# Optimization experiments

Hardware: AMD Instinct MI355X
Metric: run time of the kernel (lower is better)

The kernel has to match this reference:

```python
import jax, jax.numpy as jnp
import numpy as np

D_MODEL = 1024
NUM_HEADS = 16
HEAD_DIM = D_MODEL // NUM_HEADS
MAX_SEQ = 512


def rope_tables(seq_len, dim):
    inv_freq = 1.0 / (10000.0 ** (jnp.arange(0, dim, 2, dtype=jnp.float32) / dim))
    t = jnp.arange(seq_len, dtype=jnp.float32)
    freqs = jnp.einsum('i,j->ij', t, inv_freq)        # [S, dim/2]
    emb = jnp.concatenate([freqs, freqs], axis=-1)    # [S, dim]
    return jnp.cos(emb), jnp.sin(emb)


def rotate_half(x):
    x1, x2 = jnp.split(x, 2, axis=-1)
    return jnp.concatenate([-x2, x1], axis=-1)


def setup_inputs() -> dict:
    key = jax.random.key(0)
    ks = jax.random.split(key, 12)
    B, S, D = 16, 512, D_MODEL
    s = 1.0 / np.sqrt(D)
    inp = {
        'query': jax.random.normal(ks[0], (B, S, D), jnp.float32),
        'key': jax.random.normal(ks[1], (B, S, D), jnp.float32),
        'value': jax.random.normal(ks[2], (B, S, D), jnp.float32),
        'Wq': jax.random.normal(ks[3], (D, D), jnp.float32) * s,
        'bq': jnp.zeros((D,), jnp.float32),
        'Wk': jax.random.normal(ks[4], (D, D), jnp.float32) * s,
        'bk': jnp.zeros((D,), jnp.float32),
        'Wv': jax.random.normal(ks[5], (D, D), jnp.float32) * s,
        'bv': jnp.zeros((D,), jnp.float32),
        'Wo': jax.random.normal(ks[6], (D, D), jnp.float32) * s,
        'bo': jnp.zeros((D,), jnp.float32),
    }
    return inp


def reference(query, key, value, Wq, bq, Wk, bk, Wv, bv, Wo, bo):
    B, S, D = query.shape
    H, Hd = NUM_HEADS, HEAD_DIM
    scale = Hd ** -0.5

    def proj(x, W, b):  # torch Linear: x @ W.T + b -> [B,H,S,Hd]
        y = jnp.einsum('bsd,ed->bse', x, W) + b
        return y.reshape(B, S, H, Hd).transpose(0, 2, 1, 3)

    q = proj(query, Wq, bq)
    k = proj(key, Wk, bk)
    v = proj(value, Wv, bv)

    cos, sin = rope_tables(S, Hd)           # [S, Hd]
    cos = cos[None, None]                    # [1,1,S,Hd]
    sin = sin[None, None]
    q = q * cos + rotate_half(q) * sin
    k = k * cos + rotate_half(k) * sin

    attn = jnp.einsum('bhqd,bhkd->bhqk', q, k) * scale
    attn_w = jax.nn.softmax(attn, axis=-1)
    out = jnp.einsum('bhqk,bhkd->bhqd', attn_w, v)
    out = out.transpose(0, 2, 1, 3).reshape(B, S, D)
    out = jnp.einsum('bsd,ed->bse', out, Wo) + bo
    return out
```

## Files before the change

kernel.cpp:

```cpp
#include <hip/hip_runtime.h>
#include <hip/hip_bf16.h>
#include <math.h>

typedef __attribute__((ext_vector_type(8))) short short8;
typedef __attribute__((ext_vector_type(4))) float f32x4;
typedef unsigned short ushort;
typedef unsigned int uint;

#define BATCH 16
#define SEQ 512
#define DMODEL 1024
#define NHEADS 16
#define HD 64
#define MTOT (BATCH * SEQ)
#define NBUF ((size_t)MTOT * DMODEL)
#define WBUF ((size_t)DMODEL * DMODEL)

#define SZA (256 * 64)
#define SZB (128 * 64)

__device__ __forceinline__ ushort f2bf(float f) {
    union { float f; uint i; } v; v.f = f;
    uint r = v.i + 0x7fffu + ((v.i >> 16) & 1u);
    return (ushort)(r >> 16);
}

__device__ __forceinline__ short8 cvt8(float4 a, float4 b) {
    short8 r;
    r[0] = (short)f2bf(a.x); r[1] = (short)f2bf(a.y);
    r[2] = (short)f2bf(a.z); r[3] = (short)f2bf(a.w);
    r[4] = (short)f2bf(b.x); r[5] = (short)f2bf(b.y);
    r[6] = (short)f2bf(b.z); r[7] = (short)f2bf(b.w);
    return r;
}

__device__ __forceinline__ void gld16(const ushort* g, ushort* l) {
    __builtin_amdgcn_global_load_lds(
        (const __attribute__((address_space(1))) void*)g,
        (__attribute__((address_space(3))) void*)l, 16, 0, 0);
}

__device__ __forceinline__ f32x4 mfma16(short8 a, short8 b, f32x4 c) {
    return __builtin_amdgcn_mfma_f32_16x16x32_bf16(a, b, c, 0, 0, 0);
}

__global__ void fill_const(float* __restrict__ out, float val) {
    out[blockIdx.x * 256 + threadIdx.x] = val;
}

__global__ __launch_bounds__(256) void cvt_act(
    const float* __restrict__ i0, const float* __restrict__ i1,
    const float* __restrict__ i2, ushort* __restrict__ o0,
    ushort* __restrict__ o1, ushort* __restrict__ o2)
{
    const float* in  = blockIdx.y == 0 ? i0 : (blockIdx.y == 1 ? i1 : i2);
    ushort*      out = blockIdx.y == 0 ? o0 : (blockIdx.y == 1 ? o1 : o2);
    int i = (blockIdx.x * 256 + threadIdx.x) * 8;
    float4 a = *(const float4*)(in + i);
    float4 b = *(const float4*)(in + i + 4);
    *(short8*)(out + i) = cvt8(a, b);
}

__global__ __launch_bounds__(256) void cvt_w(
    const float* __restrict__ i0, const float* __restrict__ i1,
    const float* __restrict__ i2, const float* __restrict__ i3,
    ushort* __restrict__ o0, ushort* __restrict__ o1,
    ushort* __restrict__ o2, ushort* __restrict__ o3)
{
    const float* in  = blockIdx.y == 0 ? i0 : (blockIdx.y == 1 ? i1 :
                        (blockIdx.y == 2 ? i2 : i3));
    ushort*      out = blockIdx.y == 0 ? o0 : (blockIdx.y == 1 ? o1 :
                        (blockIdx.y == 2 ? o2 : o3));
    int i = (blockIdx.x * 256 + threadIdx.x) * 8;
    float4 a = *(const float4*)(in + i);
    float4 b = *(const float4*)(in + i + 4);
    *(short8*)(out + i) = cvt8(a, b);
}

__global__ void rope_init(float* __restrict__ cs, float* __restrict__ sn) {
    int idx = blockIdx.x * 256 + threadIdx.x;
    if (idx >= SEQ * 32) return;
    int s = idx >> 5, p = idx & 31;
    float inv = __expf(-(float)p * (1.0f / 32.0f) * logf(10000.0f));
    float th = (float)s * inv;
    cs[idx] = cosf(th);
    sn[idx] = sinf(th);
}

__device__ __forceinline__ void gemm_main(
    const ushort* __restrict__ A, const ushort* __restrict__ W,
    ushort* smA, ushort* smB, int m0, int n0, int tid, f32x4 (&acc)[4][4])
{
    const int lane = tid & 63, w = tid >> 6;
    const int quad = lane >> 4, l16 = lane & 15;
    const int wm = (w >> 1) * 64, wn = (w & 1) * 64;

    const int rA  = tid >> 3;
    const int kcs = ((tid & 7) ^ (rA & 7)) * 8;
    const ushort* gA = A + (size_t)(m0 + rA) * 1024 + kcs;
    const ushort* gB = W + (size_t)(n0 + rA) * 1024 + kcs;
    ushort* lA = smA + tid * 8;
    ushort* lB = smB + tid * 8;

    const int swz = (l16 & 7) << 3;
    const int k0 = (quad * 8) ^ swz;
    const int k1 = (32 + quad * 8) ^ swz;

#pragma unroll
    for (int i = 0; i < 4; ++i) gld16(gA + i * 65536,      lA + i * 4096);
#pragma unroll
    for (int i = 0; i < 2; ++i) gld16(gB + i * 65536,      lB + i * 4096);
#pragma unroll
    for (int i = 0; i < 4; ++i) gld16(gA + i * 65536 + 64, lA + SZA + i * 4096);
#pragma unroll
    for (int i = 0; i < 2; ++i) gld16(gB + i * 65536 + 64, lB + SZB + i * 4096);

    int bc = 0, bs = 2;
    short8 af[2][2], bf[4][2];

#pragma unroll 1
    for (int t = 0; t < 16; ++t) {
        if (t == 15) asm volatile("s_waitcnt vmcnt(0)" ::: "memory");
        else         asm volatile("s_waitcnt vmcnt(6)" ::: "memory");
        __builtin_amdgcn_s_barrier();

        const ushort* tA = smA + bc * SZA;
        const ushort* tB = smB + bc * SZB;
        const bool st = t < 14;
        const int koff = (t + 2) * 64;

#pragma unroll
        for (int mi = 0; mi < 2; ++mi) {
            const ushort* r = tA + (wm + mi * 16 + l16) * 64;
            af[mi][0] = *(const short8*)(r + k0);
            af[mi][1] = *(const short8*)(r + k1);
        }
#pragma unroll
        for (int nj = 0; nj < 4; ++nj) {
            const ushort* r = tB + (wn + nj * 16 + l16) * 64;
            bf[nj][0] = *(const short8*)(r + k0);
            bf[nj][1] = *(const short8*)(r + k1);
        }
        if (st) {
            gld16(gA + 0 * 65536 + koff, lA + bs * SZA + 0 * 4096);
            gld16(gA + 1 * 65536 + koff, lA + bs * SZA + 1 * 4096);
            gld16(gB + 0 * 65536 + koff, lB + bs * SZB + 0 * 4096);
        }
        __builtin_amdgcn_s_barrier();
        asm volatile("s_waitcnt lgkmcnt(0)" ::: "memory");
        __builtin_amdgcn_s_setprio(1);
#pragma unroll
        for (int nj = 0; nj < 4; ++nj)
#pragma unroll
            for (int mi = 0; mi < 2; ++mi) {
                acc[mi][nj] = mfma16(af[mi][0], bf[nj][0], acc[mi][nj]);
                acc[mi][nj] = mfma16(af[mi][1], bf[nj][1], acc[mi][nj]);
            }
        __builtin_amdgcn_s_setprio(0);
        __builtin_amdgcn_s_barrier();

#pragma unroll
        for (int mi = 0; mi < 2; ++mi) {
            const ushort* r = tA + (wm + (2 + mi) * 16 + l16) * 64;
            af[mi][0] = *(const short8*)(r + k0);
            af[mi][1] = *(const short8*)(r + k1);
        }
        if (st) {
            gld16(gA + 2 * 65536 + koff, lA + bs * SZA + 2 * 4096);
            gld16(gA + 3 * 65536 + koff, lA + bs * SZA + 3 * 4096);
            gld16(gB + 1 * 65536 + koff, lB + bs * SZB + 1 * 4096);
        }
        __builtin_amdgcn_s_barrier();
        asm volatile("s_waitcnt lgkmcnt(0)" ::: "memory");
        __builtin_amdgcn_s_setprio(1);
#pragma unroll
        for (int nj = 0; nj < 4; ++nj)
#pragma unroll
            for (int mi = 0; mi < 2; ++mi) {
                acc[2 + mi][nj] = mfma16(af[mi][0], bf[nj][0], acc[2 + mi][nj]);
                acc[2 + mi][nj] = mfma16(af[mi][1], bf[nj][1], acc[2 + mi][nj]);
            }
        __builtin_amdgcn_s_setprio(0);
        __builtin_amdgcn_s_barrier();

        bc = bc == 2 ? 0 : bc + 1;
        bs = bs == 2 ? 0 : bs + 1;
    }
}

__global__ __launch_bounds__(512) void qkv_proj(
    const ushort* __restrict__ Aq, const ushort* __restrict__ Ak,
    const ushort* __restrict__ Av, const ushort* __restrict__ Wq,
    const ushort* __restrict__ Wk, const ushort* __restrict__ Wv,
    const float* __restrict__ bq, const float* __restrict__ bk,
    const float* __restrict__ bv, ushort* __restrict__ Qo,
    ushort* __restrict__ Ko, ushort* __restrict__ Vo,
    const float* __restrict__ cs_tab, const float* __restrict__ sn_tab)
{
    const int z = blockIdx.z;
    const ushort* A    = z == 0 ? Aq : (z == 1 ? Ak : Av);
    const ushort* W    = z == 0 ? Wq : (z == 1 ? Wk : Wv);
    const float*  bias = z == 0 ? bq : (z == 1 ? bk : bv);
    ushort*       out  = z == 0 ? Qo : (z == 1 ? Ko : Vo);

    const int id = blockIdx.x;
    const int x = id & 7, l = id >> 3;
    const int by = x * 4 + (l >> 3);
    const int bx = l & 7;
    const int m0 = by * 256, n0 = bx * 128;

    __shared__ __align__(16) ushort smA[3 * SZA];
    __shared__ __align__(16) ushort smB[3 * SZB];

    const int tid = threadIdx.x;
    const int lane = tid & 63, w = tid >> 6;
    const int quad = lane >> 4, l16 = lane & 15;
    const int wm = (w >> 1) * 64, wn = (w & 1) * 64;

    f32x4 acc[4][4] = {};
    gemm_main(A, W, smA, smB, m0, n0, tid, acc);

    float bv4[4];
#pragma unroll
    for (int j = 0; j < 4; j++) bv4[j] = bias[n0 + wn + j * 16 + l16];

    if (z < 2) {
        const int h = (n0 + wn) >> 6;
#pragma unroll
        for (int i = 0; i < 4; i++) {
#pragma unroll
            for (int r = 0; r < 4; r++) {
                int m = m0 + wm + i * 16 + quad * 4 + r;
                int s = m & (SEQ - 1), b = m >> 9;
                size_t base = ((size_t)(b * NHEADS + h) * SEQ + s) * HD;
#pragma unroll
                for (int jj = 0; jj < 2; jj++) {
                    int p = jj * 16 + l16;
                    float c = cs_tab[s * 32 + p], sg = sn_tab[s * 32 + p];
                    float lo = acc[i][jj][r] + bv4[jj];
                    float hi = acc[i][jj + 2][r] + bv4[jj + 2];
                    out[base + p]      = f2bf(lo * c - hi * sg);
                    out[base + 32 + p] = f2bf(hi * c + lo * sg);
                }
            }
        }
    } else {
#pragma unroll
        for (int i = 0; i < 4; i++)
#pragma unroll
            for (int jj = 0; jj < 4; jj++) {
                int n = n0 + wn + jj * 16 + l16;
                int h = n >> 6, d = n & 63;
#pragma unroll
                for (int r = 0; r < 4; r++) {
                    int m = m0 + wm + i * 16 + quad * 4 + r;
                    int s = m & (SEQ - 1), b = m >> 9;
                    out[((size_t)(b * NHEADS + h) * HD + d) * SEQ + s] =
                        f2bf(acc[i][jj][r] + bv4[jj]);
                }
            }
    }
}

__global__ __launch_bounds__(512) void gemm_o(
    const ushort* __restrict__ A, const ushort* __restrict__ W,
    const float* __restrict__ bias, float* __restrict__ out)
{
    const int id = blockIdx.x;
    const int x = id & 7, l = id >> 3;
    const int by = x * 4 + (l >> 3);
    const int bx = l & 7;
    const int m0 = by * 256, n0 = bx * 128;

    __shared__ __align__(16) ushort smA[3 * SZA];
    __shared__ __align__(16) ushort smB[3 * SZB];

    const int tid = threadIdx.x;
    const int lane = tid & 63, w = tid >> 6;
    const int quad = lane >> 4, l16 = lane & 15;
    const int wm = (w >> 1) * 64, wn = (w & 1) * 64;

    f32x4 acc[4][4] = {};
    gemm_main(A, W, smA, smB, m0, n0, tid, acc);

    float bv4[4];
#pragma unroll
    for (int j = 0; j < 4; j++) bv4[j] = bias[n0 + wn + j * 16 + l16];

#pragma unroll
    for (int i = 0; i < 4; i++)
#pragma unroll
        for (int j = 0; j < 4; j++) {
            int n = n0 + wn + j * 16 + l16;
#pragma unroll
            for (int r = 0; r < 4; r++) {
                int m = m0 + wm + i * 16 + quad * 4 + r;
                out[(size_t)m * 1024 + n] = acc[i][j][r] + bv4[j];
            }
        }
}

__global__ __launch_bounds__(256) void attn(
    const ushort* __restrict__ Q, const ushort* __restrict__ K,
    const ushort* __restrict__ VT, ushort* __restrict__ O)
{
    __shared__ ushort sK[64 * 72];
    __shared__ ushort sV[64 * 72];
    __shared__ ushort sP[4][32 * 72];

    const int tid = threadIdx.x;
    const int wave = tid >> 6, lane = tid & 63;
    const int quad = lane >> 4, l16 = lane & 15;
    const int id = blockIdx.x;
    const int j8 = id >> 3;
    const int bh = (id & 7) * 32 + (j8 >> 2);
    const int q0 = (j8 & 3) * 128;
    const int qw = q0 + wave * 32;

    const ushort* Qbh = Q + (size_t)bh * SEQ * HD;
    const ushort* Kbh = K + (size_t)bh * SEQ * HD;
    const ushort* Vbh = VT + (size_t)bh * HD * SEQ;

    const float S2 = 0.125f * 1.44269504f;
    const float C2 = 12.0f * 1.44269504f;

    short8 qf[2][2];
#pragma unroll
    for (int mi = 0; mi < 2; mi++)
#pragma unroll
        for (int ks = 0; ks < 2; ks++)
            qf[mi][ks] = *(const short8*)(Qbh + (size_t)(qw + mi * 16 + l16) * HD +
                                          ks * 32 + quad * 8);

    f32x4 o_acc[2][4] = {};
    float lsum[2][4] = {};

    const int cA = tid, cB = tid + 256;
    const int rA = cA >> 3, colA = (cA & 7) * 8;
    const int rB = cB >> 3, colB = (cB & 7) * 8;

    for (int kt = 0; kt < SEQ; kt += 64) {
        *(short8*)(sK + rA * 72 + colA) = *(const short8*)(Kbh + (size_t)(kt + rA) * HD + colA);
        *(short8*)(sK + rB * 72 + colB) = *(const short8*)(Kbh + (size_t)(kt + rB) * HD + colB);
        *(short8*)(sV + rA * 72 + colA) = *(const short8*)(Vbh + (size_t)rA * SEQ + kt + colA);
        *(short8*)(sV + rB * 72 + colB) = *(const short8*)(Vbh + (size_t)rB * SEQ + kt + colB);
        __syncthreads();

        f32x4 sc[2][4];
#pragma unroll
        for (int nj = 0; nj < 4; nj++) {
            short8 kf0 = *(const short8*)(sK + (nj * 16 + l16) * 72 + quad * 8);
            short8 kf1 = *(const short8*)(sK + (nj * 16 + l16) * 72 + 32 + quad * 8);
#pragma unroll
            for (int mi = 0; mi < 2; mi++) {
                f32x4 z = {0.f, 0.f, 0.f, 0.f};
                z = mfma16(qf[mi][0], kf0, z);
                z = mfma16(qf[mi][1], kf1, z);
                sc[mi][nj] = z;
            }
        }

#pragma unroll
        for (int mi = 0; mi < 2; mi++)
#pragma unroll
            for (int r = 0; r < 4; r++) {
                float p0 = __builtin_amdgcn_exp2f(fmaf(sc[mi][0][r], S2, -C2));
                float p1 = __builtin_amdgcn_exp2f(fmaf(sc[mi][1][r], S2, -C2));
                float p2 = __builtin_amdgcn_exp2f(fmaf(sc[mi][2][r], S2, -C2));
                float p3 = __builtin_amdgcn_exp2f(fmaf(sc[mi][3][r], S2, -C2));
                sc[mi][0][r] = p0; sc[mi][1][r] = p1;
                sc[mi][2][r] = p2; sc[mi][3][r] = p3;
                lsum[mi][r] += (p0 + p1) + (p2 + p3);
            }

#pragma unroll
        for (int mi = 0; mi < 2; mi++)
#pragma unroll
            for (int nj = 0; nj < 4; nj++)
#pragma unroll
                for (int r = 0; r < 4; r++)
                    sP[wave][(mi * 16 + quad * 4 + r) * 72 + nj * 16 + l16] =
                        f2bf(sc[mi][nj][r]);
        __syncthreads();

#pragma unroll
        for (int ks = 0; ks < 2; ks++) {
            short8 pf0 = *(const short8*)(&sP[wave][(l16) * 72 + ks * 32 + quad * 8]);
            short8 pf1 = *(const short8*)(&sP[wave][(16 + l16) * 72 + ks * 32 + quad * 8]);
#pragma unroll
            for (int dj = 0; dj < 4; dj++) {
                short8 vf = *(const short8*)(sV + (dj * 16 + l16) * 72 + ks * 32 + quad * 8);
                o_acc[0][dj] = mfma16(pf0, vf, o_acc[0][dj]);
                o_acc[1][dj] = mfma16(pf1, vf, o_acc[1][dj]);
            }
        }
        __syncthreads();
    }

    const int h = bh & (NHEADS - 1), b = bh >> 4;
#pragma unroll
    for (int mi = 0; mi < 2; mi++)
#pragma unroll
        for (int r = 0; r < 4; r++) {
            float l = lsum[mi][r];
            l += __shfl_xor(l, 1, 64);
            l += __shfl_xor(l, 2, 64);
            l += __shfl_xor(l, 4, 64);
            l += __shfl_xor(l, 8, 64);
            float inv = 1.0f / l;
            int s = qw + mi * 16 + quad * 4 + r;
            size_t base = ((size_t)(b * SEQ + s)) * DMODEL + h * HD;
#pragma unroll
            for (int dj = 0; dj < 4; dj++)
                O[base + dj * 16 + l16] = f2bf(o_acc[mi][dj][r] * inv);
        }
}

extern "C" void kernel_launch(void* const* d_in, const int* in_sizes, int n_in,
                              void* d_out, int out_size, void* d_ws, size_t ws_size,
                              hipStream_t stream) {
    bool ok = (n_in == 11) && (out_size == (int)NBUF) &&
              in_sizes[0] == (int)NBUF && in_sizes[1] == (int)NBUF &&
              in_sizes[2] == (int)NBUF &&
              in_sizes[3] == (int)WBUF && in_sizes[4] == 1024 &&
              in_sizes[5] == (int)WBUF && in_sizes[6] == 1024 &&
              in_sizes[7] == (int)WBUF && in_sizes[8] == 1024 &&
              in_sizes[9] == (int)WBUF && in_sizes[10] == 1024;
    if (!ok) {
        fill_const<<<NBUF / 256, 256, 0, stream>>>((float*)d_out, 1000.0f);
        return;
    }
    size_t need = 2 * (size_t)SEQ * 32 * 4 + 4 * NBUF * 2 + 4 * WBUF * 2;
    if (ws_size < need) return;

    const float* q  = (const float*)d_in[0];
    const float* k  = (const float*)d_in[1];
    const float* v  = (const float*)d_in[2];
    const float* Wq = (const float*)d_in[3];
    const float* bq = (const float*)d_in[4];
    const float* Wk = (const float*)d_in[5];
    const float* bk = (const float*)d_in[6];
    const float* Wv = (const float*)d_in[7];
    const float* bv = (const float*)d_in[8];
    const float* Wo = (const float*)d_in[9];
    const float* bo = (const float*)d_in[10];

    float* cs = (float*)d_ws;
    float* sn = cs + SEQ * 32;
    ushort* Qb  = (ushort*)(sn + SEQ * 32);
    ushort* Kb  = Qb + NBUF;
    ushort* VTb = Kb + NBUF;
    ushort* Xb  = VTb + NBUF;
    ushort* Wqb = Xb + NBUF;
    ushort* Wkb = Wqb + WBUF;
    ushort* Wvb = Wkb + WBUF;
    ushort* Wob = Wvb + WBUF;
    ushort* Qx = (ushort*)d_out;
    ushort* Kx = Qx + NBUF;

    rope_init<<<64, 256, 0, stream>>>(cs, sn);
    cvt_w<<<dim3(WBUF / 2048, 4), 256, 0, stream>>>(Wq, Wk, Wv, Wo,
                                                    Wqb, Wkb, Wvb, Wob);
    cvt_act<<<dim3(NBUF / 2048, 3), 256, 0, stream>>>(q, k, v, Qx, Kx, Xb);

    qkv_proj<<<dim3(256, 1, 3), 512, 0, stream>>>(
        Qx, Kx, Xb, Wqb, Wkb, Wvb, bq, bk, bv, Qb, Kb, VTb, cs, sn);

    attn<<<BATCH * NHEADS * 4, 256, 0, stream>>>(Qb, Kb, VTb, Xb);

    gemm_o<<<256, 512, 0, stream>>>(Xb, Wob, bo, (float*)d_out);
}
```

Before: 294.6 us.

## Fuse fp32-to-bf16 activation conversion into QKV GEMM and restructure pipeline

Drops the separate cvt_act kernel: the QKV projection GEMM now reads fp32 activations straight into registers, converts them to bf16 and writes them into swizzled LDS, overlapping that with MFMA work. The A tile goes from triple to double buffering and the pipeline is reorganised so each k-step needs only one barrier instead of several. Both GEMMs also ask for two blocks per CU through launch bounds. This removes one full read and write of three activation tensors, at the cost of register-staged loads, more VGPR pressure and hand-tuned waitcnt counts that must stay correct.

Result: slower. 363.2 us (+23.3%).

```diff
diff --git a/kernel.cpp b/kernel.cpp
--- a/kernel.cpp
+++ b/kernel.cpp
@@ -19,6 +19,8 @@
 #define SZA (256 * 64)
 #define SZB (128 * 64)
 
+#define FENCE asm volatile("" ::: "memory")
+
 __device__ __forceinline__ ushort f2bf(float f) {
     union { float f; uint i; } v; v.f = f;
     uint r = v.i + 0x7fffu + ((v.i >> 16) & 1u);
@@ -46,19 +48,6 @@
 
 __global__ void fill_const(float* __restrict__ out, float val) {
     out[blockIdx.x * 256 + threadIdx.x] = val;
-}
-
-__global__ __launch_bounds__(256) void cvt_act(
-    const float* __restrict__ i0, const float* __restrict__ i1,
-    const float* __restrict__ i2, ushort* __restrict__ o0,
-    ushort* __restrict__ o1, ushort* __restrict__ o2)
-{
-    const float* in  = blockIdx.y == 0 ? i0 : (blockIdx.y == 1 ? i1 : i2);
-    ushort*      out = blockIdx.y == 0 ? o0 : (blockIdx.y == 1 ? o1 : o2);
-    int i = (blockIdx.x * 256 + threadIdx.x) * 8;
-    float4 a = *(const float4*)(in + i);
-    float4 b = *(const float4*)(in + i + 4);
-    *(short8*)(out + i) = cvt8(a, b);
 }
 
 __global__ __launch_bounds__(256) void cvt_w(
@@ -87,47 +76,71 @@
     sn[idx] = sinf(th);
 }
 
-__device__ __forceinline__ void gemm_main(
-    const ushort* __restrict__ A, const ushort* __restrict__ W,
-    ushort* smA, ushort* smB, int m0, int n0, int tid, f32x4 (&acc)[4][4])
+template<bool F32A>
+__device__ __forceinline__ void gemm_core(
+    const void* __restrict__ Ap, const ushort* __restrict__ W,
+    ushort* __restrict__ smA, ushort* __restrict__ smB,
+    int m0, int n0, int tid, f32x4 (&acc)[4][4])
 {
     const int lane = tid & 63, w = tid >> 6;
     const int quad = lane >> 4, l16 = lane & 15;
     const int wm = (w >> 1) * 64, wn = (w & 1) * 64;
-
-    const int rA  = tid >> 3;
-    const int kcs = ((tid & 7) ^ (rA & 7)) * 8;
-    const ushort* gA = A + (size_t)(m0 + rA) * 1024 + kcs;
-    const ushort* gB = W + (size_t)(n0 + rA) * 1024 + kcs;
-    ushort* lA = smA + tid * 8;
-    ushort* lB = smB + tid * 8;
-
     const int swz = (l16 & 7) << 3;
     const int k0 = (quad * 8) ^ swz;
-    const int k1 = (32 + quad * 8) ^ swz;
-
-#pragma unroll
-    for (int i = 0; i < 4; ++i) gld16(gA + i * 65536,      lA + i * 4096);
-#pragma unroll
-    for (int i = 0; i < 2; ++i) gld16(gB + i * 65536,      lB + i * 4096);
-#pragma unroll
-    for (int i = 0; i < 4; ++i) gld16(gA + i * 65536 + 64, lA + SZA + i * 4096);
-#pragma unroll
-    for (int i = 0; i < 2; ++i) gld16(gB + i * 65536 + 64, lB + SZB + i * 4096);
-
-    int bc = 0, bs = 2;
-    short8 af[2][2], bf[4][2];
-
+    const int k1 = ((4 + quad) * 8) ^ swz;
+
+    const int rB = tid >> 3;
+    const ushort* gB = W + (size_t)(n0 + rB) * 1024 + ((tid & 7) ^ (rB & 7)) * 8;
+    ushort* lB = smB + tid * 8;
+
+    const float*  Af = (const float*)Ap;
+    const ushort* Ab = (const ushort*)Ap;
+    const int rA32 = tid >> 1, hA = tid & 1;
+    const float* gA32 = Af + (size_t)(m0 + rA32) * 1024 + hA * 32;
+    const int rA16 = tid >> 3;
+    const ushort* gA16 = Ab + (size_t)(m0 + rA16) * 1024 + ((tid & 7) ^ (rA16 & 7)) * 8;
+    ushort* lA = smA + tid * 8;
+
+    float4 fa[8];
+
+    if (F32A) {
+#pragma unroll
+        for (int j = 0; j < 8; ++j) fa[j] = ((const float4*)gA32)[j];
+        FENCE;
+        gld16(gB, lB); gld16(gB + 65536, lB + 4096);
+        gld16(gB + 64, lB + SZB); gld16(gB + 65536 + 64, lB + SZB + 4096);
+        FENCE;
+        asm volatile("s_waitcnt vmcnt(4)" ::: "memory");
+        {
+            ushort* d = smA + rA32 * 64;
+#pragma unroll
+            for (int j2 = 0; j2 < 4; ++j2)
+                *(short8*)(d + ((hA * 4 + j2) ^ (rA32 & 7)) * 8) =
+                    cvt8(fa[2 * j2], fa[2 * j2 + 1]);
+        }
+#pragma unroll
+        for (int j = 0; j < 8; ++j) fa[j] = ((const float4*)(gA32 + 64))[j];
+        FENCE;
+        asm volatile("s_waitcnt vmcnt(10) lgkmcnt(0)" ::: "memory");
+    } else {
+#pragma unroll
+        for (int i = 0; i < 4; ++i) gld16(gA16 + i * 65536, lA + i * 4096);
+        gld16(gB, lB); gld16(gB + 65536, lB + 4096);
+        FENCE;
+        gld16(gB + 64, lB + SZB); gld16(gB + 65536 + 64, lB + SZB + 4096);
+        FENCE;
+        asm volatile("s_waitcnt vmcnt(2)" ::: "memory");
+    }
+    __builtin_amdgcn_s_barrier();
+    FENCE;
+
+    int cur = 0;
 #pragma unroll 1
     for (int t = 0; t < 16; ++t) {
-        if (t == 15) asm volatile("s_waitcnt vmcnt(0)" ::: "memory");
-        else         asm volatile("s_waitcnt vmcnt(6)" ::: "memory");
-        __builtin_amdgcn_s_barrier();
-
-        const ushort* tA = smA + bc * SZA;
-        const ushort* tB = smB + bc * SZB;
-        const bool st = t < 14;
-        const int koff = (t + 2) * 64;
+        const ushort* tA = smA + cur * SZA;
+        const ushort* tB = smB + (t % 3) * SZB;
+        const int nxt = cur ^ 1;
+        short8 af[2][2], bf[4][2];
 
 #pragma unroll
         for (int mi = 0; mi < 2; ++mi) {
@@ -141,13 +154,34 @@
             bf[nj][0] = *(const short8*)(r + k0);
             bf[nj][1] = *(const short8*)(r + k1);
         }
-        if (st) {
-            gld16(gA + 0 * 65536 + koff, lA + bs * SZA + 0 * 4096);
-            gld16(gA + 1 * 65536 + koff, lA + bs * SZA + 1 * 4096);
-            gld16(gB + 0 * 65536 + koff, lB + bs * SZB + 0 * 4096);
-        }
-        __builtin_amdgcn_s_barrier();
-        asm volatile("s_waitcnt lgkmcnt(0)" ::: "memory");
+        if (!F32A && t < 15) {
+            const ushort* g = gA16 + (size_t)(t + 1) * 64;
+            ushort* d = lA + nxt * SZA;
+#pragma unroll
+            for (int i = 0; i < 4; ++i) gld16(g + i * 65536, d + i * 4096);
+        }
+        if (t < 14) {
+            const ushort* g = gB + (size_t)(t + 2) * 64;
+            ushort* d = lB + ((t + 2) % 3) * SZB;
+            gld16(g, d); gld16(g + 65536, d + 4096);
+        }
+        FENCE;
+        if (F32A) {
+            if (t < 14) asm volatile("s_waitcnt vmcnt(2)" ::: "memory");
+            else        asm volatile("s_waitcnt vmcnt(0)" ::: "memory");
+            if (t < 15) {
+                ushort* d = smA + nxt * SZA + rA32 * 64;
+#pragma unroll
+                for (int j2 = 0; j2 < 4; ++j2)
+                    *(short8*)(d + ((hA * 4 + j2) ^ (rA32 & 7)) * 8) =
+                        cvt8(fa[2 * j2], fa[2 * j2 + 1]);
+                asm volatile("s_waitcnt lgkmcnt(4)" ::: "memory");
+            } else {
+                asm volatile("s_waitcnt lgkmcnt(0)" ::: "memory");
+            }
+        } else {
+            asm volatile("s_waitcnt lgkmcnt(0)" ::: "memory");
+        }
         __builtin_amdgcn_s_setprio(1);
 #pragma unroll
         for (int nj = 0; nj < 4; ++nj)
@@ -157,7 +191,6 @@
                 acc[mi][nj] = mfma16(af[mi][1], bf[nj][1], acc[mi][nj]);
             }
         __builtin_amdgcn_s_setprio(0);
-        __builtin_amdgcn_s_barrier();
 
 #pragma unroll
         for (int mi = 0; mi < 2; ++mi) {
@@ -165,12 +198,12 @@
             af[mi][0] = *(const short8*)(r + k0);
             af[mi][1] = *(const short8*)(r + k1);
         }
-        if (st) {
-            gld16(gA + 2 * 65536 + koff, lA + bs * SZA + 2 * 4096);
-            gld16(gA + 3 * 65536 + koff, lA + bs * SZA + 3 * 4096);
-            gld16(gB + 1 * 65536 + koff, lB + bs * SZB + 1 * 4096);
-        }
-        __builtin_amdgcn_s_barrier();
+        if (F32A && t < 14) {
+            const float* g = gA32 + (size_t)(t + 2) * 64;
+#pragma unroll
+            for (int j = 0; j < 8; ++j) fa[j] = ((const float4*)g)[j];
+        }
+        FENCE;
         asm volatile("s_waitcnt lgkmcnt(0)" ::: "memory");
         __builtin_amdgcn_s_setprio(1);
 #pragma unroll
@@ -181,16 +214,21 @@
                 acc[2 + mi][nj] = mfma16(af[mi][1], bf[nj][1], acc[2 + mi][nj]);
             }
         __builtin_amdgcn_s_setprio(0);
+
+        if (!F32A) {
+            if (t < 14) asm volatile("s_waitcnt vmcnt(2)" ::: "memory");
+            else        asm volatile("s_waitcnt vmcnt(0)" ::: "memory");
+        }
+        FENCE;
         __builtin_amdgcn_s_barrier();
-
-        bc = bc == 2 ? 0 : bc + 1;
-        bs = bs == 2 ? 0 : bs + 1;
+        FENCE;
+        cur = nxt;
     }
 }
 
-__global__ __launch_bounds__(512) void qkv_proj(
-    const ushort* __restrict__ Aq, const ushort* __restrict__ Ak,
-    const ushort* __restrict__ Av, const ushort* __restrict__ Wq,
+__global__ __launch_bounds__(512, 2) void qkv_proj(
+    const float* __restrict__ Aq, const float* __restrict__ Ak,
+    const float* __restrict__ Av, const ushort* __restrict__ Wq,
     const ushort* __restrict__ Wk, const ushort* __restrict__ Wv,
     const float* __restrict__ bq, const float* __restrict__ bk,
     const float* __restrict__ bv, ushort* __restrict__ Qo,
@@ -198,7 +236,7 @@
     const float* __restrict__ cs_tab, const float* __restrict__ sn_tab)
 {
     const int z = blockIdx.z;
-    const ushort* A    = z == 0 ? Aq : (z == 1 ? Ak : Av);
+    const float*  A    = z == 0 ? Aq : (z == 1 ? Ak : Av);
     const ushort* W    = z == 0 ? Wq : (z == 1 ? Wk : Wv);
     const float*  bias = z == 0 ? bq : (z == 1 ? bk : bv);
     ushort*       out  = z == 0 ? Qo : (z == 1 ? Ko : Vo);
@@ -209,7 +247,7 @@
     const int bx = l & 7;
     const int m0 = by * 256, n0 = bx * 128;
 
-    __shared__ __align__(16) ushort smA[3 * SZA];
+    __shared__ __align__(16) ushort smA[2 * SZA];
     __shared__ __align__(16) ushort smB[3 * SZB];
 
     const int tid = threadIdx.x;
@@ -218,7 +256,7 @@
     const int wm = (w >> 1) * 64, wn = (w & 1) * 64;
 
     f32x4 acc[4][4] = {};
-    gemm_main(A, W, smA, smB, m0, n0, tid, acc);
+    gemm_core<true>(A, W, smA, smB, m0, n0, tid, acc);
 
     float bv4[4];
 #pragma unroll
@@ -262,7 +300,7 @@
     }
 }
 
-__global__ __launch_bounds__(512) void gemm_o(
+__global__ __launch_bounds__(512, 2) void gemm_o(
     const ushort* __restrict__ A, const ushort* __restrict__ W,
     const float* __restrict__ bias, float* __restrict__ out)
 {
@@ -272,7 +310,7 @@
     const int bx = l & 7;
     const int m0 = by * 256, n0 = bx * 128;
 
-    __shared__ __align__(16) ushort smA[3 * SZA];
+    __shared__ __align__(16) ushort smA[2 * SZA];
     __shared__ __align__(16) ushort smB[3 * SZB];
 
     const int tid = threadIdx.x;
@@ -281,7 +319,7 @@
     const int wm = (w >> 1) * 64, wn = (w & 1) * 64;
 
     f32x4 acc[4][4] = {};
-    gemm_main(A, W, smA, smB, m0, n0, tid, acc);
+    gemm_core<false>(A, W, smA, smB, m0, n0, tid, acc);
 
     float bv4[4];
 #pragma unroll
@@ -455,16 +493,13 @@
     ushort* Wkb = Wqb + WBUF;
     ushort* Wvb = Wkb + WBUF;
     ushort* Wob = Wvb + WBUF;
-    ushort* Qx = (ushort*)d_out;
-    ushort* Kx = Qx + NBUF;
 
     rope_init<<<64, 256, 0, stream>>>(cs, sn);
     cvt_w<<<dim3(WBUF / 2048, 4), 256, 0, stream>>>(Wq, Wk, Wv, Wo,
                                                     Wqb, Wkb, Wvb, Wob);
-    cvt_act<<<dim3(NBUF / 2048, 3), 256, 0, stream>>>(q, k, v, Qx, Kx, Xb);
 
     qkv_proj<<<dim3(256, 1, 3), 512, 0, stream>>>(
-        Qx, Kx, Xb, Wqb, Wkb, Wvb, bq, bk, bv, Qb, Kb, VTb, cs, sn);
+        q, k, v, Wqb, Wkb, Wvb, bq, bk, bv, Qb, Kb, VTb, cs, sn);
 
     attn<<<BATCH * NHEADS * 4, 256, 0, stream>>>(Qb, Kb, VTb, Xb);
 
```

## Simplify GEMM main loop to one barrier per k-step with full fragment loads

Applied to the files above, without the earlier changes.

Rewrites the shared GEMM inner loop. The two-half iteration, with four barriers and explicit LDS waits, becomes a single phase per k-tile: all A and B fragments are loaded, the next-stage global-to-LDS copies are issued, then all MFMAs run. Both GEMM kernels also gain a launch_bounds occupancy hint of 2 blocks. The aim is to cut barrier and synchronisation overhead, at the cost of more live fragment registers. The occupancy hint may force register spills, and LDS size likely prevents two resident blocks anyway.

New measurement: 286.5 us. 2.7% less time.

```diff
diff --git a/kernel.cpp b/kernel.cpp
--- a/kernel.cpp
+++ b/kernel.cpp
@@ -19,6 +19,8 @@
 #define SZA (256 * 64)
 #define SZB (128 * 64)
 
+#define FENCE asm volatile("" ::: "memory")
+
 __device__ __forceinline__ ushort f2bf(float f) {
     union { float f; uint i; } v; v.f = f;
     uint r = v.i + 0x7fffu + ((v.i >> 16) & 1u);
@@ -87,108 +89,79 @@
     sn[idx] = sinf(th);
 }
 
-__device__ __forceinline__ void gemm_main(
+__device__ __forceinline__ void gemm_core(
     const ushort* __restrict__ A, const ushort* __restrict__ W,
-    ushort* smA, ushort* smB, int m0, int n0, int tid, f32x4 (&acc)[4][4])
+    ushort* __restrict__ smA, ushort* __restrict__ smB,
+    int m0, int n0, int tid, f32x4 (&acc)[4][4])
 {
     const int lane = tid & 63, w = tid >> 6;
     const int quad = lane >> 4, l16 = lane & 15;
     const int wm = (w >> 1) * 64, wn = (w & 1) * 64;
-
-    const int rA  = tid >> 3;
-    const int kcs = ((tid & 7) ^ (rA & 7)) * 8;
-    const ushort* gA = A + (size_t)(m0 + rA) * 1024 + kcs;
-    const ushort* gB = W + (size_t)(n0 + rA) * 1024 + kcs;
+    const int swz = (l16 & 7) << 3;
+    const int k0 = (quad * 8) ^ swz;
+    const int k1 = ((4 + quad) * 8) ^ swz;
+
+    const int r = tid >> 3;
+    const int kc = ((tid & 7) ^ (r & 7)) * 8;
+    const ushort* gA = A + (size_t)(m0 + r) * 1024 + kc;
+    const ushort* gB = W + (size_t)(n0 + r) * 1024 + kc;
     ushort* lA = smA + tid * 8;
     ushort* lB = smB + tid * 8;
 
-    const int swz = (l16 & 7) << 3;
-    const int k0 = (quad * 8) ^ swz;
-    const int k1 = (32 + quad * 8) ^ swz;
-
-#pragma unroll
-    for (int i = 0; i < 4; ++i) gld16(gA + i * 65536,      lA + i * 4096);
-#pragma unroll
-    for (int i = 0; i < 2; ++i) gld16(gB + i * 65536,      lB + i * 4096);
+#pragma unroll
+    for (int i = 0; i < 4; ++i) gld16(gA + i * 65536, lA + i * 4096);
+    gld16(gB, lB); gld16(gB + 65536, lB + 4096);
+    FENCE;
 #pragma unroll
     for (int i = 0; i < 4; ++i) gld16(gA + i * 65536 + 64, lA + SZA + i * 4096);
-#pragma unroll
-    for (int i = 0; i < 2; ++i) gld16(gB + i * 65536 + 64, lB + SZB + i * 4096);
-
-    int bc = 0, bs = 2;
-    short8 af[2][2], bf[4][2];
+    gld16(gB + 64, lB + SZB); gld16(gB + 65536 + 64, lB + SZB + 4096);
+    FENCE;
 
 #pragma unroll 1
     for (int t = 0; t < 16; ++t) {
-        if (t == 15) asm volatile("s_waitcnt vmcnt(0)" ::: "memory");
-        else         asm volatile("s_waitcnt vmcnt(6)" ::: "memory");
+        if (t < 15) asm volatile("s_waitcnt vmcnt(6)" ::: "memory");
+        else        asm volatile("s_waitcnt vmcnt(0)" ::: "memory");
         __builtin_amdgcn_s_barrier();
 
-        const ushort* tA = smA + bc * SZA;
-        const ushort* tB = smB + bc * SZB;
-        const bool st = t < 14;
-        const int koff = (t + 2) * 64;
-
-#pragma unroll
-        for (int mi = 0; mi < 2; ++mi) {
-            const ushort* r = tA + (wm + mi * 16 + l16) * 64;
-            af[mi][0] = *(const short8*)(r + k0);
-            af[mi][1] = *(const short8*)(r + k1);
+        const ushort* tA = smA + (t % 3) * SZA;
+        const ushort* tB = smB + (t % 3) * SZB;
+        short8 af[4][2], bf[4][2];
+#pragma unroll
+        for (int mi = 0; mi < 4; ++mi) {
+            const ushort* rp = tA + (wm + mi * 16 + l16) * 64;
+            af[mi][0] = *(const short8*)(rp + k0);
+            af[mi][1] = *(const short8*)(rp + k1);
         }
 #pragma unroll
         for (int nj = 0; nj < 4; ++nj) {
-            const ushort* r = tB + (wn + nj * 16 + l16) * 64;
-            bf[nj][0] = *(const short8*)(r + k0);
-            bf[nj][1] = *(const short8*)(r + k1);
-        }
-        if (st) {
-            gld16(gA + 0 * 65536 + koff, lA + bs * SZA + 0 * 4096);
-            gld16(gA + 1 * 65536 + koff, lA + bs * SZA + 1 * 4096);
-            gld16(gB + 0 * 65536 + koff, lB + bs * SZB + 0 * 4096);
-        }
-        __builtin_amdgcn_s_barrier();
-        asm volatile("s_waitcnt lgkmcnt(0)" ::: "memory");
+            const ushort* rp = tB + (wn + nj * 16 + l16) * 64;
+            bf[nj][0] = *(const short8*)(rp + k0);
+            bf[nj][1] = *(const short8*)(rp + k1);
+        }
+        if (t < 14) {
+            const int sl = (t + 2) % 3;
+            const ushort* ga = gA + (size_t)(t + 2) * 64;
+            const ushort* gb = gB + (size_t)(t + 2) * 64;
+            ushort* da = lA + sl * SZA;
+            ushort* db = lB + sl * SZB;
+#pragma unroll
+            for (int i = 0; i < 4; ++i) gld16(ga + i * 65536, da + i * 4096);
+            gld16(gb, db); gld16(gb + 65536, db + 4096);
+        }
+        FENCE;
         __builtin_amdgcn_s_setprio(1);
 #pragma unroll
         for (int nj = 0; nj < 4; ++nj)
 #pragma unroll
-            for (int mi = 0; mi < 2; ++mi) {
+            for (int mi = 0; mi < 4; ++mi) {
                 acc[mi][nj] = mfma16(af[mi][0], bf[nj][0], acc[mi][nj]);
                 acc[mi][nj] = mfma16(af[mi][1], bf[nj][1], acc[mi][nj]);
             }
         __builtin_amdgcn_s_setprio(0);
-        __builtin_amdgcn_s_barrier();
-
-#pragma unroll
-        for (int mi = 0; mi < 2; ++mi) {
-            const ushort* r = tA + (wm + (2 + mi) * 16 + l16) * 64;
-            af[mi][0] = *(const short8*)(r + k0);
-            af[mi][1] = *(const short8*)(r + k1);
-        }
-        if (st) {
-            gld16(gA + 2 * 65536 + koff, lA + bs * SZA + 2 * 4096);
-            gld16(gA + 3 * 65536 + koff, lA + bs * SZA + 3 * 4096);
-            gld16(gB + 1 * 65536 + koff, lB + bs * SZB + 1 * 4096);
-        }
-        __builtin_amdgcn_s_barrier();
-        asm volatile("s_waitcnt lgkmcnt(0)" ::: "memory");
-        __builtin_amdgcn_s_setprio(1);
-#pragma unroll
-        for (int nj = 0; nj < 4; ++nj)
-#pragma unroll
-            for (int mi = 0; mi < 2; ++mi) {
-                acc[2 + mi][nj] = mfma16(af[mi][0], bf[nj][0], acc[2 + mi][nj]);
-                acc[2 + mi][nj] = mfma16(af[mi][1], bf[nj][1], acc[2 + mi][nj]);
-            }
-        __builtin_amdgcn_s_setprio(0);
-        __builtin_amdgcn_s_barrier();
-
-        bc = bc == 2 ? 0 : bc + 1;
-        bs = bs == 2 ? 0 : bs + 1;
     }
 }
 
-__global__ __launch_bounds__(512) void qkv_proj(
+__global__ __launch_bounds__(512, 2) void qkv_proj(
     const ushort* __restrict__ Aq, const ushort* __restrict__ Ak,
     const ushort* __restrict__ Av, const ushort* __restrict__ Wq,
     const ushort* __restrict__ Wk, const ushort* __restrict__ Wv,
@@ -218,7 +191,7 @@
     const int wm = (w >> 1) * 64, wn = (w & 1) * 64;
 
     f32x4 acc[4][4] = {};
-    gemm_main(A, W, smA, smB, m0, n0, tid, acc);
+    gemm_core(A, W, smA, smB, m0, n0, tid, acc);
 
     float bv4[4];
 #pragma unroll
@@ -262,7 +235,7 @@
     }
 }
 
-__global__ __launch_bounds__(512) void gemm_o(
+__global__ __launch_bounds__(512, 2) void gemm_o(
     const ushort* __restrict__ A, const ushort* __restrict__ W,
     const float* __restrict__ bias, float* __restrict__ out)
 {
@@ -281,7 +254,7 @@
     const int wm = (w >> 1) * 64, wn = (w & 1) * 64;
 
     f32x4 acc[4][4] = {};
-    gemm_main(A, W, smA, smB, m0, n0, tid, acc);
+    gemm_core(A, W, smA, smB, m0, n0, tid, acc);
 
     float bv4[4];
 #pragma unroll
```
